# Optimization experiments

Hardware: AMD Instinct MI355X
Metric: run time of the kernel (lower is better)

Reference implementation:

```python
import jax, jax.numpy as jnp
import numpy as np

B, S, D, H = 4, 2048, 1024, 16
HD = D // H  # head_dim = 64


def setup_inputs() -> dict:
    key = jax.random.key(0)
    ks = jax.random.split(key, 6)
    scale = 0.02
    x = jax.random.normal(ks[0], (B, S, D), dtype=jnp.float32)
    # per-head projection weights, torch Linear is y = x @ W.T; store as [H, D, HD]
    Wq = jax.random.normal(ks[1], (H, D, HD), dtype=jnp.float32) * scale
    Wk = jax.random.normal(ks[2], (H, D, HD), dtype=jnp.float32) * scale
    Wv = jax.random.normal(ks[3], (H, D, HD), dtype=jnp.float32) * scale
    Wo = jax.random.normal(ks[4], (D, D), dtype=jnp.float32) * scale  # torch [out, in]
    bo = jax.random.normal(ks[5], (D,), dtype=jnp.float32) * scale
    return {"x": x, "Wq": Wq, "Wk": Wk, "Wv": Wv, "Wo": Wo, "bo": bo}


def reference(x, Wq, Wk, Wv, Wo, bo):
    # project: [B,S,D] x [H,D,HD] -> [B,H,S,HD]
    q = jnp.einsum("bsd,hde->bhse", x, Wq)
    k = jnp.einsum("bsd,hde->bhse", x, Wk)
    v = jnp.einsum("bsd,hde->bhse", x, Wv)
    scores = jnp.einsum("bhse,bhte->bhst", q, k) / jnp.sqrt(jnp.float32(HD))
    causal = jnp.tril(jnp.ones((S, S), dtype=bool))  # same as registered tril mask
    scores = jnp.where(causal, scores, -jnp.inf)
    w = jax.nn.softmax(scores, axis=-1)
    out = jnp.einsum("bhst,bhte->bhse", w, v)  # [B,H,S,HD]
    # concat heads along feature dim: [B,S,H*HD] = [B,S,D]
    out = out.transpose(0, 2, 1, 3).reshape(B, S, D)
    # output projection: torch Linear y = x @ W.T + b
    return jnp.einsum("bsd,od->bso", out, Wo) + bo
```

## Files before the change

kernel.cpp:

```cpp
#include <hip/hip_runtime.h>
#include <hip/hip_bf16.h>

typedef __bf16 bf16x8 __attribute__((ext_vector_type(8)));
typedef float f32x4 __attribute__((ext_vector_type(4)));
typedef unsigned short u16x4 __attribute__((ext_vector_type(4)));
typedef unsigned short u16x8 __attribute__((ext_vector_type(8)));
typedef unsigned uint4v __attribute__((ext_vector_type(4)));

#define B_ 4
#define S_ 2048
#define D_ 1024
#define H_ 16
#define HD_ 64

__device__ __forceinline__ unsigned short f2bf(float f) {
  unsigned u = __float_as_uint(f);
  u += 0x7fff + ((u >> 16) & 1);
  return (unsigned short)(u >> 16);
}

__device__ __forceinline__ void gload16(const void* g, void* l) {
  __builtin_amdgcn_global_load_lds((const __attribute__((address_space(1))) unsigned int*)g,
                                   (__attribute__((address_space(3))) unsigned int*)l,
                                   16, 0, 0);
}

__global__ void pack_x_k(const float* __restrict__ in, unsigned short* __restrict__ out, int n4) {
  int i = blockIdx.x * blockDim.x + threadIdx.x;
  int stride = gridDim.x * blockDim.x;
  for (; i < n4; i += stride) {
    float4 v = reinterpret_cast<const float4*>(in)[i];
    u16x4 o = {f2bf(v.x), f2bf(v.y), f2bf(v.z), f2bf(v.w)};
    reinterpret_cast<u16x4*>(out)[i] = o;
  }
}

__global__ void pack_wqkv_k(const float* __restrict__ Wq, const float* __restrict__ Wk,
                            const float* __restrict__ Wv, unsigned short* __restrict__ Wt) {
  int o = blockIdx.x * blockDim.x + threadIdx.x;
  int n = o >> 10;
  int d = o & 1023;
  const float* W = (n < 1024) ? Wq : (n < 2048) ? Wk : Wv;
  int nn = n & 1023;
  int h = nn >> 6, e = nn & 63;
  Wt[o] = f2bf(W[(h << 16) + (d << 6) + e]);
}

__global__ __launch_bounds__(512, 2) void gemm256_k(const unsigned short* __restrict__ A,
                                                    const unsigned short* __restrict__ Bt,
                                                    unsigned short* __restrict__ C,
                                                    int M, int N, int K) {
  __shared__ __align__(16) unsigned short lds[2][3][128 * 64];
  const int tid = threadIdx.x;
  const int wid = tid >> 6, lane = tid & 63;
  const int r = lane & 15, g = lane >> 4;
  const int wm = wid >> 2, wn = wid & 3;

  const int i_hw = blockIdx.y * gridDim.x + blockIdx.x;
  const int xcd = i_hw & 7, j = i_hw >> 3;
  const long arow0 = (long)((xcd & 3) * 8 + (j & 7)) * 256;
  const long bcol0 = (long)((xcd >> 2) * 12 + (j >> 3)) * 128;

  const f32x4 z4 = {0.f, 0.f, 0.f, 0.f};
  f32x4 acc[8][2];
#pragma unroll
  for (int m = 0; m < 8; ++m)
#pragma unroll
    for (int n = 0; n < 2; ++n) acc[m][n] = z4;

  auto stage_half = [&](int kt, int which) {
    const unsigned short* src = (which == 2) ? Bt + bcol0 * K : A + (arow0 + 128 * which) * K;
    const int k0 = kt << 6;
    unsigned short* base = &lds[kt & 1][which][0];
#pragma unroll
    for (int c = 0; c < 2; ++c) {
      const int jj = c * 512 + tid;
      const int row = jj >> 3, cc = jj & 7;
      const int ccs = cc ^ (row & 7);
      gload16(src + (long)row * K + k0 + ccs * 8, base + jj * 8);
    }
  };

  bf16x8 af[4][2], bv[2][2];
  auto read_a = [&](int buf, int mh) {
#pragma unroll
    for (int i2 = 0; i2 < 4; ++i2)
#pragma unroll
      for (int kk = 0; kk < 2; ++kk) {
        const int rowh = (2 * i2 + wm) * 16 + r;
        af[i2][kk] = *(const bf16x8*)&lds[buf][mh][rowh * 64 + (((kk << 2) + g) ^ (rowh & 7)) * 8];
      }
  };
  auto read_b = [&](int buf) {
#pragma unroll
    for (int j2 = 0; j2 < 2; ++j2)
#pragma unroll
      for (int kk = 0; kk < 2; ++kk) {
        const int rowh = (4 * j2 + wn) * 16 + r;
        bv[j2][kk] = *(const bf16x8*)&lds[buf][2][rowh * 64 + (((kk << 2) + g) ^ (rowh & 7)) * 8];
      }
  };
  auto mma_h = [&](int mh) {
    __builtin_amdgcn_s_setprio(1);
#pragma unroll
    for (int kk = 0; kk < 2; ++kk)
#pragma unroll
      for (int i2 = 0; i2 < 4; ++i2)
#pragma unroll
        for (int j2 = 0; j2 < 2; ++j2)
          acc[4 * mh + i2][j2] = __builtin_amdgcn_mfma_f32_16x16x32_bf16(
              af[i2][kk], bv[j2][kk], acc[4 * mh + i2][j2], 0, 0, 0);
    __builtin_amdgcn_s_setprio(0);
  };

  const int nk = K >> 6;
  stage_half(0, 0);
  stage_half(0, 2);
  stage_half(0, 1);
  asm volatile("s_waitcnt vmcnt(2)" ::: "memory");
  asm volatile("s_barrier" ::: "memory");

  for (int t = 0; t < nk; ++t) {
    const int buf = t & 1;
    const bool pre = (t + 1 < nk);
    read_a(buf, 0);
    read_b(buf);
    if (pre) { stage_half(t + 1, 0); stage_half(t + 1, 2); }
    asm volatile("s_barrier" ::: "memory");
    mma_h(0);
    if (pre) asm volatile("s_waitcnt vmcnt(4)" ::: "memory");
    else     asm volatile("s_waitcnt vmcnt(0)" ::: "memory");
    asm volatile("s_waitcnt lgkmcnt(0)\n\ts_barrier" ::: "memory");
    read_a(buf, 1);
    if (pre) stage_half(t + 1, 1);
    asm volatile("s_barrier" ::: "memory");
    mma_h(1);
    if (pre) asm volatile("s_waitcnt vmcnt(2)" ::: "memory");
    asm volatile("s_waitcnt lgkmcnt(0)\n\ts_barrier" ::: "memory");
  }

#pragma unroll
  for (int m = 0; m < 8; ++m)
#pragma unroll
    for (int n = 0; n < 2; ++n)
#pragma unroll
      for (int rr = 0; rr < 4; ++rr) {
        const long row = arow0 + (2 * m + wm) * 16 + g * 4 + rr;
        const long col = bcol0 + (4 * n + wn) * 16 + r;
        C[row * N + col] = f2bf(acc[m][n][rr]);
      }
}

__global__ __launch_bounds__(256, 2) void gemm_bt_k(const unsigned short* __restrict__ A,
                                                    const unsigned short* __restrict__ Bt,
                                                    float* __restrict__ C,
                                                    const float* __restrict__ bias,
                                                    int M, int N, int K) {
  __shared__ __align__(16) unsigned short lA[2][128 * 64];
  __shared__ __align__(16) unsigned short lB[2][128 * 64];
  const int tid = threadIdx.x;
  const int wid = tid >> 6, lane = tid & 63;
  const int r = lane & 15, g = lane >> 4;
  const long arow0 = (long)blockIdx.x * 128;
  const long brow0 = (long)blockIdx.y * 128;
  const int wr = (wid >> 1) * 64, wc = (wid & 1) * 64;

  const f32x4 z4 = {0.f, 0.f, 0.f, 0.f};
  f32x4 acc[4][4];
#pragma unroll
  for (int m = 0; m < 4; ++m)
#pragma unroll
    for (int n = 0; n < 4; ++n) acc[m][n] = z4;

  auto stage = [&](int buf, int k0) {
#pragma unroll
    for (int c = 0; c < 4; ++c) {
      const int j = c * 256 + wid * 64 + lane;
      const int row = j >> 3, col = (j & 7) * 8;
      gload16(A + (arow0 + row) * K + k0 + col, &lA[buf][(c * 256 + wid * 64) * 8]);
      gload16(Bt + (brow0 + row) * K + k0 + col, &lB[buf][(c * 256 + wid * 64) * 8]);
    }
  };

  stage(0, 0);
  __syncthreads();
  const int nk = K >> 6;
  for (int kt = 0; kt < nk; ++kt) {
    const int cur = kt & 1;
    if (kt + 1 < nk) stage(cur ^ 1, (kt + 1) << 6);
#pragma unroll
    for (int kk = 0; kk < 2; ++kk) {
      bf16x8 af[4], bfr[4];
#pragma unroll
      for (int m = 0; m < 4; ++m)
        af[m] = *(const bf16x8*)&lA[cur][(wr + m * 16 + r) * 64 + kk * 32 + g * 8];
#pragma unroll
      for (int n = 0; n < 4; ++n)
        bfr[n] = *(const bf16x8*)&lB[cur][(wc + n * 16 + r) * 64 + kk * 32 + g * 8];
#pragma unroll
      for (int m = 0; m < 4; ++m)
#pragma unroll
        for (int n = 0; n < 4; ++n)
          acc[m][n] = __builtin_amdgcn_mfma_f32_16x16x32_bf16(af[m], bfr[n], acc[m][n], 0, 0, 0);
    }
    __syncthreads();
  }

#pragma unroll
  for (int m = 0; m < 4; ++m) {
#pragma unroll
    for (int n = 0; n < 4; ++n) {
#pragma unroll
      for (int rr = 0; rr < 4; ++rr) {
        const long row = arow0 + wr + m * 16 + g * 4 + rr;
        const long col = brow0 + wc + n * 16 + r;
        C[row * N + col] = acc[m][n][rr] + bias[col];
      }
    }
  }
}

__global__ __launch_bounds__(256, 3) void attn_k(const unsigned short* __restrict__ qkv,
                                                 unsigned short* __restrict__ out) {
  __shared__ __align__(16) unsigned short lK[2][64 * 64];
  __shared__ __align__(16) unsigned short lVt[2][64 * 64];

  const int tid = threadIdx.x, wid = tid >> 6, lane = tid & 63;
  const int r = lane & 15, g = lane >> 4;
  const int bh = blockIdx.x;
  const int b = bh >> 4, h = bh & 15;
  const int qb = 15 - (int)blockIdx.y;
  const int q0 = qb * 128;

  const long base = ((long)b * S_) * 3072 + h * 64;
  const unsigned short* Qg = qkv + base;
  const unsigned short* Kg = qkv + base + 1024;
  const unsigned short* Vg = qkv + base + 2048;

  int qrow[2];
  bf16x8 qf[2][2];
#pragma unroll
  for (int qs = 0; qs < 2; ++qs) {
    qrow[qs] = q0 + qs * 64 + wid * 16 + r;
#pragma unroll
    for (int kk = 0; kk < 2; ++kk)
      qf[qs][kk] = *(const bf16x8*)&Qg[(long)qrow[qs] * 3072 + kk * 32 + g * 8];
  }

  const f32x4 z4 = {0.f, 0.f, 0.f, 0.f};
  f32x4 o[2][4];
#pragma unroll
  for (int qs = 0; qs < 2; ++qs)
#pragma unroll
    for (int nt = 0; nt < 4; ++nt) o[qs][nt] = z4;
  float m_i[2] = {-1e30f, -1e30f};
  float l_i[2] = {0.f, 0.f};

  u16x8 kreg[2], vreg[2];
  auto load_regs = [&](int t0) {
#pragma unroll
    for (int c = 0; c < 2; ++c) {
      const int j = c * 256 + tid;
      const int tt = j >> 3, e0 = (j & 7) * 8;
      kreg[c] = *(const u16x8*)&Kg[(long)(t0 + tt) * 3072 + e0];
      const int tc = j & 63, ec = j >> 6;
      vreg[c] = *(const u16x8*)&Vg[(long)(t0 + tc) * 3072 + ec * 8];
    }
  };
  auto write_lds = [&](int buf) {
#pragma unroll
    for (int c = 0; c < 2; ++c) {
      const int j = c * 256 + tid;
      const int row = j >> 3, cc = j & 7;
      *(u16x8*)&lK[buf][(row * 8 + (cc ^ (row & 7))) * 8] = kreg[c];
      const int tc = j & 63, ec = j >> 6;
#pragma unroll
      for (int i = 0; i < 8; ++i) {
        const int e = ec * 8 + i;
        lVt[buf][e * 64 + (tc ^ (i * 8))] = vreg[c][i];
      }
    }
  };

  const int ntiles = (q0 >> 6) + 2;
  load_regs(0);
  write_lds(0);

  for (int t = 0; t < ntiles; ++t) {
    const int cur = t & 1;
    if (t + 1 < ntiles) load_regs((t + 1) << 6);
    __syncthreads();

    const int t0 = t << 6;
    const bool act0 = (t < ntiles - 1);
    const bool diag0 = (t == ntiles - 2);
    const bool diag1 = (t == ntiles - 1);

    f32x4 st[2][4];
#pragma unroll
    for (int tt = 0; tt < 4; ++tt) { st[0][tt] = z4; st[1][tt] = z4; }
    __builtin_amdgcn_s_setprio(1);
#pragma unroll
    for (int kk = 0; kk < 2; ++kk)
#pragma unroll
      for (int tt = 0; tt < 4; ++tt) {
        const int row = tt * 16 + r, cc = kk * 4 + g;
        bf16x8 kf = *(const bf16x8*)&lK[cur][(row * 8 + (cc ^ (row & 7))) * 8];
        st[1][tt] = __builtin_amdgcn_mfma_f32_16x16x32_bf16(kf, qf[1][kk], st[1][tt], 0, 0, 0);
        if (act0)
          st[0][tt] = __builtin_amdgcn_mfma_f32_16x16x32_bf16(kf, qf[0][kk], st[0][tt], 0, 0, 0);
      }
    __builtin_amdgcn_s_setprio(0);

    bf16x8 pf[2][2];
    unsigned corr_bits[2] = {0x3f800000u, 0x3f800000u};
    bool dodef[2] = {true, true};
#pragma unroll
    for (int qs = 0; qs < 2; ++qs) {
      if (qs == 0 && !act0) continue;
      const bool diag = qs ? diag1 : diag0;
      float sv[16];
#pragma unroll
      for (int tt = 0; tt < 4; ++tt)
#pragma unroll
        for (int rg = 0; rg < 4; ++rg) {
          float s = st[qs][tt][rg];
          if (diag && (t0 + tt * 16 + g * 4 + rg > qrow[qs])) s = -1e30f;
          sv[tt * 4 + rg] = s;
        }
      float h0 = fmaxf(fmaxf(fmaxf(sv[0], sv[1]), fmaxf(sv[2], sv[3])),
                       fmaxf(fmaxf(sv[4], sv[5]), fmaxf(sv[6], sv[7])));
      float h1 = fmaxf(fmaxf(fmaxf(sv[8], sv[9]), fmaxf(sv[10], sv[11])),
                       fmaxf(fmaxf(sv[12], sv[13]), fmaxf(sv[14], sv[15])));
      const float pmax = fmaxf(h0, h1);
      const bool defer = __all(pmax - m_i[qs] <= 64.f);
      float corr = 1.f;
      if (!defer) {
        float mx = fmaxf(pmax, m_i[qs]);
        mx = fmaxf(mx, __shfl_xor(mx, 16, 64));
        mx = fmaxf(mx, __shfl_xor(mx, 32, 64));
        corr = __expf((m_i[qs] - mx) * 0.125f);
        m_i[qs] = mx;
      }
      dodef[qs] = defer;
      corr_bits[qs] = __float_as_uint(corr);
      const float m8 = m_i[qs] * 0.125f;
      float p[16];
      float rs = 0.f;
#pragma unroll
      for (int i = 0; i < 16; ++i) {
        p[i] = __expf(__builtin_fmaf(sv[i], 0.125f, -m8));
        rs += p[i];
      }
      rs += __shfl_xor(rs, 16, 64);
      rs += __shfl_xor(rs, 32, 64);
      l_i[qs] = l_i[qs] * corr + rs;
      unsigned cw[4][2];
#pragma unroll
      for (int tt = 0; tt < 4; ++tt)
#pragma unroll
        for (int e = 0; e < 2; ++e)
          asm("v_cvt_pk_bf16_f32 %0, %1, %2"
              : "=v"(cw[tt][e]) : "v"(p[tt * 4 + 2 * e]), "v"(p[tt * 4 + 2 * e + 1]));
#pragma unroll
      for (int kk = 0; kk < 2; ++kk) {
        unsigned x0 = cw[2 * kk][0], y0 = cw[2 * kk + 1][0];
        unsigned x1 = cw[2 * kk][1], y1 = cw[2 * kk + 1][1];
        asm volatile("v_permlane32_swap_b32 %0, %1" : "+v"(x0), "+v"(y0));
        asm volatile("v_permlane16_swap_b32 %0, %1" : "+v"(x0), "+v"(y0));
        asm volatile("v_permlane32_swap_b32 %0, %1" : "+v"(x1), "+v"(y1));
        asm volatile("v_permlane16_swap_b32 %0, %1" : "+v"(x1), "+v"(y1));
        uint4v w = {x0, x1, y0, y1};
        pf[qs][kk] = *(bf16x8*)&w;
      }
    }
#pragma unroll
    for (int qs = 0; qs < 2; ++qs) {
      if (qs == 0 && !act0) continue;
      if (!dodef[qs]) {
        const float corr = __uint_as_float(corr_bits[qs]);
#pragma unroll
        for (int rr = 0; rr < 4; ++rr) {
          const float c = __shfl(corr, g * 4 + rr, 64);
#pragma unroll
          for (int nt = 0; nt < 4; ++nt) o[qs][nt][rr] *= c;
        }
      }
    }

    __builtin_amdgcn_s_setprio(1);
#pragma unroll
    for (int kk = 0; kk < 2; ++kk)
#pragma unroll
      for (int nt = 0; nt < 4; ++nt) {
        const int row = nt * 16 + r, cc = kk * 4 + g;
        const bf16x8 vf = *(const bf16x8*)&lVt[cur][(row * 8 + (cc ^ (row & 7))) * 8];
        o[1][nt] = __builtin_amdgcn_mfma_f32_16x16x32_bf16(pf[1][kk], vf, o[1][nt], 0, 0, 0);
        if (act0)
          o[0][nt] = __builtin_amdgcn_mfma_f32_16x16x32_bf16(pf[0][kk], vf, o[0][nt], 0, 0, 0);
      }
    __builtin_amdgcn_s_setprio(0);

    if (t + 1 < ntiles) write_lds(cur ^ 1);
  }

#pragma unroll
  for (int qs = 0; qs < 2; ++qs) {
    float linv[4];
#pragma unroll
    for (int rr = 0; rr < 4; ++rr)
      linv[rr] = 1.f / __shfl(l_i[qs], g * 4 + rr, 64);
#pragma unroll
    for (int nt = 0; nt < 4; ++nt)
#pragma unroll
      for (int rr = 0; rr < 4; ++rr) {
        const long s = q0 + qs * 64 + wid * 16 + g * 4 + rr;
        out[((long)b * S_ + s) * 1024 + h * 64 + nt * 16 + r] = f2bf(o[qs][nt][rr] * linv[rr]);
      }
  }
}

extern "C" void kernel_launch(void* const* d_in, const int* in_sizes, int n_in,
                              void* d_out, int out_size, void* d_ws, size_t ws_size,
                              hipStream_t stream) {
  const float* x = (const float*)d_in[0];
  const float* Wq = (const float*)d_in[1];
  const float* Wk = (const float*)d_in[2];
  const float* Wv = (const float*)d_in[3];
  const float* Wo = (const float*)d_in[4];
  const float* bo = (const float*)d_in[5];
  float* out = (float*)d_out;

  char* ws = (char*)d_ws;
  unsigned short* Xb = (unsigned short*)(ws);
  unsigned short* Wt = (unsigned short*)(ws + (16ul << 20));
  unsigned short* Wob = (unsigned short*)(ws + (22ul << 20));
  unsigned short* QKV = (unsigned short*)(ws + (24ul << 20));
  unsigned short* AO = (unsigned short*)(ws + (72ul << 20));

  pack_x_k<<<2048, 256, 0, stream>>>(x, Xb, (B_ * S_ * D_) / 4);
  pack_x_k<<<512, 256, 0, stream>>>(Wo, Wob, (D_ * D_) / 4);
  pack_wqkv_k<<<(3 * D_ * D_) / 256, 256, 0, stream>>>(Wq, Wk, Wv, Wt);

  gemm256_k<<<dim3(32, 24), 512, 0, stream>>>(Xb, Wt, QKV, B_ * S_, 3 * D_, D_);
  attn_k<<<dim3(64, 16), 256, 0, stream>>>(QKV, AO);
  gemm_bt_k<<<dim3(64, 8), 256, 0, stream>>>(AO, Wob, out, bo, B_ * S_, D_, D_);
}
```

Baseline: 194.5 us.

## Write V transposed from QKV GEMM and stage K/V via direct global-to-LDS loads

The QKV projection epilogue now writes Q and K to a packed [B*S,2048] buffer and writes V pre-transposed per head as [B,H,64,S]. This lets the attention kernel stage both K and V tiles with direct global-to-LDS 16-byte loads, dropping the register round-trip and the scalar per-element transposed LDS writes. The cost is strided 8-byte scattered stores in the GEMM epilogue for the V part. Attention launch bounds also drop from 3 to 2 blocks per SM.

```diff
diff --git a/kernel.cpp b/kernel.cpp
--- a/kernel.cpp
+++ b/kernel.cpp
@@ -48,7 +48,8 @@
 
 __global__ __launch_bounds__(512, 2) void gemm256_k(const unsigned short* __restrict__ A,
                                                     const unsigned short* __restrict__ Bt,
-                                                    unsigned short* __restrict__ C,
+                                                    unsigned short* __restrict__ QK,
+                                                    unsigned short* __restrict__ VT,
                                                     int M, int N, int K) {
   __shared__ __align__(16) unsigned short lds[2][3][128 * 64];
   const int tid = threadIdx.x;
@@ -139,16 +140,33 @@
     asm volatile("s_waitcnt lgkmcnt(0)\n\ts_barrier" ::: "memory");
   }
 
-#pragma unroll
-  for (int m = 0; m < 8; ++m)
-#pragma unroll
-    for (int n = 0; n < 2; ++n)
-#pragma unroll
-      for (int rr = 0; rr < 4; ++rr) {
-        const long row = arow0 + (2 * m + wm) * 16 + g * 4 + rr;
-        const long col = bcol0 + (4 * n + wn) * 16 + r;
-        C[row * N + col] = f2bf(acc[m][n][rr]);
-      }
+  if (bcol0 < 2048) {
+#pragma unroll
+    for (int m = 0; m < 8; ++m)
+#pragma unroll
+      for (int n = 0; n < 2; ++n)
+#pragma unroll
+        for (int rr = 0; rr < 4; ++rr) {
+          const long row = arow0 + (2 * m + wm) * 16 + g * 4 + rr;
+          const long col = bcol0 + (4 * n + wn) * 16 + r;
+          QK[row * 2048 + col] = f2bf(acc[m][n][rr]);
+        }
+  } else {
+#pragma unroll
+    for (int m = 0; m < 8; ++m) {
+      const long row0 = arow0 + (2 * m + wm) * 16 + g * 4;
+      const long b = row0 >> 11, s = row0 & 2047;
+#pragma unroll
+      for (int n = 0; n < 2; ++n) {
+        const long vcol = bcol0 - 2048 + (4 * n + wn) * 16 + r;
+        const long h = vcol >> 6, e = vcol & 63;
+        u16x4 w4;
+#pragma unroll
+        for (int rr = 0; rr < 4; ++rr) w4[rr] = f2bf(acc[m][n][rr]);
+        *(u16x4*)&VT[(((b << 4) + h) * 64 + e) * 2048 + s] = w4;
+      }
+    }
+  }
 }
 
 __global__ __launch_bounds__(256, 2) void gemm_bt_k(const unsigned short* __restrict__ A,
@@ -220,7 +238,8 @@
   }
 }
 
-__global__ __launch_bounds__(256, 3) void attn_k(const unsigned short* __restrict__ qkv,
+__global__ __launch_bounds__(256, 2) void attn_k(const unsigned short* __restrict__ qk,
+                                                 const unsigned short* __restrict__ vt,
                                                  unsigned short* __restrict__ out) {
   __shared__ __align__(16) unsigned short lK[2][64 * 64];
   __shared__ __align__(16) unsigned short lVt[2][64 * 64];
@@ -232,10 +251,9 @@
   const int qb = 15 - (int)blockIdx.y;
   const int q0 = qb * 128;
 
-  const long base = ((long)b * S_) * 3072 + h * 64;
-  const unsigned short* Qg = qkv + base;
-  const unsigned short* Kg = qkv + base + 1024;
-  const unsigned short* Vg = qkv + base + 2048;
+  const unsigned short* Qg = qk + ((long)b * S_) * 2048 + h * 64;
+  const unsigned short* Kg = Qg + 1024;
+  const unsigned short* Vg = vt + ((long)(b * 16 + h)) * 64 * 2048;
 
   int qrow[2];
   bf16x8 qf[2][2];
@@ -244,7 +262,7 @@
     qrow[qs] = q0 + qs * 64 + wid * 16 + r;
 #pragma unroll
     for (int kk = 0; kk < 2; ++kk)
-      qf[qs][kk] = *(const bf16x8*)&Qg[(long)qrow[qs] * 3072 + kk * 32 + g * 8];
+      qf[qs][kk] = *(const bf16x8*)&Qg[(long)qrow[qs] * 2048 + kk * 32 + g * 8];
   }
 
   const f32x4 z4 = {0.f, 0.f, 0.f, 0.f};
@@ -256,40 +274,24 @@
   float m_i[2] = {-1e30f, -1e30f};
   float l_i[2] = {0.f, 0.f};
 
-  u16x8 kreg[2], vreg[2];
-  auto load_regs = [&](int t0) {
-#pragma unroll
-    for (int c = 0; c < 2; ++c) {
-      const int j = c * 256 + tid;
-      const int tt = j >> 3, e0 = (j & 7) * 8;
-      kreg[c] = *(const u16x8*)&Kg[(long)(t0 + tt) * 3072 + e0];
-      const int tc = j & 63, ec = j >> 6;
-      vreg[c] = *(const u16x8*)&Vg[(long)(t0 + tc) * 3072 + ec * 8];
-    }
-  };
-  auto write_lds = [&](int buf) {
+  auto stage = [&](int buf, int t0) {
 #pragma unroll
     for (int c = 0; c < 2; ++c) {
       const int j = c * 256 + tid;
       const int row = j >> 3, cc = j & 7;
-      *(u16x8*)&lK[buf][(row * 8 + (cc ^ (row & 7))) * 8] = kreg[c];
-      const int tc = j & 63, ec = j >> 6;
-#pragma unroll
-      for (int i = 0; i < 8; ++i) {
-        const int e = ec * 8 + i;
-        lVt[buf][e * 64 + (tc ^ (i * 8))] = vreg[c][i];
-      }
+      const int ccs = (cc ^ (row & 7)) << 3;
+      gload16(Kg + (long)(t0 + row) * 2048 + ccs, &lK[buf][j * 8]);
+      gload16(Vg + (long)row * 2048 + t0 + ccs, &lVt[buf][j * 8]);
     }
   };
 
   const int ntiles = (q0 >> 6) + 2;
-  load_regs(0);
-  write_lds(0);
+  stage(0, 0);
 
   for (int t = 0; t < ntiles; ++t) {
     const int cur = t & 1;
-    if (t + 1 < ntiles) load_regs((t + 1) << 6);
     __syncthreads();
+    if (t + 1 < ntiles) stage(cur ^ 1, (t + 1) << 6);
 
     const int t0 = t << 6;
     const bool act0 = (t < ntiles - 1);
@@ -400,8 +402,6 @@
           o[0][nt] = __builtin_amdgcn_mfma_f32_16x16x32_bf16(pf[0][kk], vf, o[0][nt], 0, 0, 0);
       }
     __builtin_amdgcn_s_setprio(0);
-
-    if (t + 1 < ntiles) write_lds(cur ^ 1);
   }
 
 #pragma unroll
@@ -435,14 +435,15 @@
   unsigned short* Xb = (unsigned short*)(ws);
   unsigned short* Wt = (unsigned short*)(ws + (16ul << 20));
   unsigned short* Wob = (unsigned short*)(ws + (22ul << 20));
-  unsigned short* QKV = (unsigned short*)(ws + (24ul << 20));
+  unsigned short* QK = (unsigned short*)(ws + (24ul << 20));
+  unsigned short* VT = (unsigned short*)(ws + (56ul << 20));
   unsigned short* AO = (unsigned short*)(ws + (72ul << 20));
 
   pack_x_k<<<2048, 256, 0, stream>>>(x, Xb, (B_ * S_ * D_) / 4);
   pack_x_k<<<512, 256, 0, stream>>>(Wo, Wob, (D_ * D_) / 4);
   pack_wqkv_k<<<(3 * D_ * D_) / 256, 256, 0, stream>>>(Wq, Wk, Wv, Wt);
 
-  gemm256_k<<<dim3(32, 24), 512, 0, stream>>>(Xb, Wt, QKV, B_ * S_, 3 * D_, D_);
-  attn_k<<<dim3(64, 16), 256, 0, stream>>>(QKV, AO);
+  gemm256_k<<<dim3(32, 24), 512, 0, stream>>>(Xb, Wt, QK, VT, B_ * S_, 3 * D_, D_);
+  attn_k<<<dim3(64, 16), 256, 0, stream>>>(QK, VT, AO);
   gemm_bt_k<<<dim3(64, 8), 256, 0, stream>>>(AO, Wob, out, bo, B_ * S_, D_, D_);
 }
```

New measurement: 192.1 us. Within noise of the previous version (-1.2%).
